# Kernel tuning notes

Measured on AMD Instinct MI355X. Metric: run time of the kernel, lower is better.

Reference implementation:

```python
import jax, jax.numpy as jnp
import numpy as np

N = 2048
NONGT = 2048
EMB = 64
GROUP = 16
FEAT = 256
DM = 1024  # dim[0] == dim[1]
DHEAD = DM // GROUP  # 64


def setup_inputs() -> dict:
    key = jax.random.key(0)
    ks = jax.random.split(key, 12)
    s = lambda fan_in: 1.0 / np.sqrt(fan_in)
    return {
        "roi_feat": jax.random.normal(ks[0], (N, FEAT), jnp.float32),
        "position_embedding": jax.random.uniform(ks[1], (N, NONGT, EMB), jnp.float32),
        "fc1_w": jax.random.normal(ks[2], (GROUP, EMB), jnp.float32) * s(EMB),
        "fc1_b": jnp.zeros((GROUP,), jnp.float32),
        "fc2_w": jax.random.normal(ks[3], (DM, FEAT), jnp.float32) * s(FEAT),
        "fc2_b": jnp.zeros((DM,), jnp.float32),
        "fc3_w": jax.random.normal(ks[4], (DM, FEAT), jnp.float32) * s(FEAT),
        "fc3_b": jnp.zeros((DM,), jnp.float32),
        "conv_w": jax.random.normal(ks[5], (FEAT, GROUP * FEAT), jnp.float32) * s(GROUP * FEAT),
        "conv_b": jnp.zeros((FEAT,), jnp.float32),
        "nongt_dim": NONGT,
    }


def reference(roi_feat, position_embedding, fc1_w, fc1_b, fc2_w, fc2_b,
              fc3_w, fc3_b, conv_w, conv_b, nongt_dim):
    nongt_roi_feat = roi_feat[:nongt_dim, :]                      # [M, FEAT]
    # position bias: relu(fc1(pe)) -> [N, M, G] -> [N, G, M]
    pos1 = jax.nn.relu(jnp.einsum('nme,ge->nmg', position_embedding, fc1_w) + fc1_b)
    aff_weight = jnp.transpose(pos1, (0, 2, 1))                   # [N, G, M]
    # grouped Q, K
    q = roi_feat @ fc2_w.T + fc2_b                                # [N, DM]
    q = q.reshape(-1, GROUP, DHEAD)                               # [N, G, d]
    k = nongt_roi_feat @ fc3_w.T + fc3_b                          # [M, DM]
    k = k.reshape(-1, GROUP, DHEAD)                               # [M, G, d]
    scale = 1.0 / np.sqrt(float(DHEAD))
    aff = jnp.einsum('ngd,mgd->ngm', q, k) * scale                # [N, G, M]
    weighted = jnp.log(jnp.maximum(aff_weight, 1e-6)) + aff
    aff_softmax = jax.nn.softmax(weighted, axis=-1)               # [N, G, M]
    out_t = jnp.einsum('ngm,mc->ngc', aff_softmax, nongt_roi_feat)  # [N, G, FEAT]
    flat = out_t.reshape(out_t.shape[0], GROUP * FEAT)            # channel order g*FEAT + c
    return flat @ conv_w.T + conv_b                               # [N, FEAT]
```

## Files before the change

### kernel.cpp

```cpp
#include <hip/hip_runtime.h>
#include <hip/hip_bf16.h>

#define NQ   2048
#define NK   2048
#define EMB  64
#define GRP  16
#define FEAT 256

typedef __bf16 bf16x8 __attribute__((ext_vector_type(8)));
typedef __bf16 bf16x4 __attribute__((ext_vector_type(4)));
typedef float  f32x4  __attribute__((ext_vector_type(4)));

#define MFMA(a, b, c) __builtin_amdgcn_mfma_f32_16x16x32_bf16((a), (b), (c), 0, 0, 0)

typedef __attribute__((address_space(3))) unsigned int  lds_u32;
typedef __attribute__((address_space(1))) unsigned int  glb_u32;

static __device__ __forceinline__ bf16x8 cvt8(float4 a, float4 b) {
    bf16x8 r;
    r[0] = (__bf16)a.x; r[1] = (__bf16)a.y; r[2] = (__bf16)a.z; r[3] = (__bf16)a.w;
    r[4] = (__bf16)b.x; r[5] = (__bf16)b.y; r[6] = (__bf16)b.z; r[7] = (__bf16)b.w;
    return r;
}

__launch_bounds__(256, 2)
__global__ void prep_all(const float* __restrict__ roi,
                         const float* __restrict__ pe,
                         const float* __restrict__ fc1w,
                         const float* __restrict__ fc1b,
                         const float* __restrict__ fc2w,
                         const float* __restrict__ fc2b,
                         const float* __restrict__ fc3w,
                         const float* __restrict__ fc3b,
                         const float* __restrict__ cw,
                         __bf16* __restrict__ roiT,
                         __bf16* __restrict__ convwb,
                         __bf16* __restrict__ qb,
                         __bf16* __restrict__ kb,
                         __bf16* __restrict__ wg) {
    __shared__ float tile[64][65];
    const int b   = blockIdx.x;
    const int tid = threadIdx.x;

    if (b < 128) {
        const int m0 = (b >> 2) * 64, c0 = (b & 3) * 64;
        const int tr = tid >> 4, tc = tid & 15;
#pragma unroll
        for (int ch = 0; ch < 4; ++ch) {
            int r = ch * 16 + tr;
            float4 v = *(const float4*)(roi + (m0 + r) * 256 + c0 + tc * 4);
            tile[r][tc * 4 + 0] = v.x; tile[r][tc * 4 + 1] = v.y;
            tile[r][tc * 4 + 2] = v.z; tile[r][tc * 4 + 3] = v.w;
        }
        __syncthreads();
#pragma unroll
        for (int ch = 0; ch < 4; ++ch) {
            int crow = ch * 16 + tr;
            int mm = tc * 4;
            bf16x4 o;
            o[0] = (__bf16)tile[mm + 0][crow]; o[1] = (__bf16)tile[mm + 1][crow];
            o[2] = (__bf16)tile[mm + 2][crow]; o[3] = (__bf16)tile[mm + 3][crow];
            *(bf16x4*)(roiT + (c0 + crow) * 2048 + m0 + mm) = o;
        }
    } else if (b < 640) {
        const int cb = b - 128;
        for (int i = cb * 256 + tid; i < 262144; i += 512 * 256) {
            float4 v = ((const float4*)cw)[i];
            bf16x4 o;
            o[0] = (__bf16)v.x; o[1] = (__bf16)v.y; o[2] = (__bf16)v.z; o[3] = (__bf16)v.w;
            ((bf16x4*)convwb)[i] = o;
        }
    } else if (b < 1664) {
        const int qi = b - 640;
        const int x  = qi & 511;
        const int isK = qi >> 9;
        const float* W    = isK ? fc3w : fc2w;
        const float* bias = isK ? fc3b : fc2b;
        __bf16*      out  = isK ? kb   : qb;
        const int l = tid & 63, wid = tid >> 6;
        const int n0 = (x >> 2) * 16;
        const int dmB = (x & 3) * 256 + wid * 64;
        const int lr = l & 15, lk = l >> 4;
        f32x4 acc[4];
#pragma unroll
        for (int i = 0; i < 4; ++i) acc[i] = (f32x4){0.f, 0.f, 0.f, 0.f};
        for (int k0 = 0; k0 < 256; k0 += 32) {
            const float* ap = roi + (n0 + lr) * 256 + k0 + lk * 8;
            bf16x8 af = cvt8(*(const float4*)ap, *(const float4*)(ap + 4));
#pragma unroll
            for (int cf = 0; cf < 4; ++cf) {
                const float* bp = W + (dmB + cf * 16 + lr) * 256 + k0 + lk * 8;
                acc[cf] = MFMA(af, cvt8(*(const float4*)bp, *(const float4*)(bp + 4)), acc[cf]);
            }
        }
#pragma unroll
        for (int cf = 0; cf < 4; ++cf) {
            int dm = dmB + cf * 16 + lr;
            float bv = bias[dm];
            int g = dm >> 6, d = dm & 63;
#pragma unroll
            for (int ri = 0; ri < 4; ++ri) {
                int n = n0 + lk * 4 + ri;
                out[(g * 2048 + n) * 64 + d] = (__bf16)(acc[cf][ri] + bv);
            }
        }
    } else {
        const int wb = b - 1664;
        const int l = tid & 63, wid = tid >> 6;
        const int lr = l & 15, lk = l >> 4;
        const long n = wb >> 2;
        const int mbase = (wb & 3) * 512 + wid * 128;

        bf16x8 fcB[2];
#pragma unroll
        for (int s = 0; s < 2; ++s) {
            const float* p = fc1w + lr * 64 + s * 32 + lk * 8;
            fcB[s] = cvt8(*(const float4*)p, *(const float4*)(p + 4));
        }
        const float bias = fc1b[lr];

        const float* pebase = pe + (n * 2048 + mbase + lr) * 64 + lk * 8;
        __bf16* obase = wg + (n * 16 + lr) * 2048 + mbase + lk * 4;

#pragma unroll 4
        for (int it = 0; it < 8; ++it) {
            const float* p0 = pebase + it * 16 * 64;
            f32x4 c = (f32x4){0.f, 0.f, 0.f, 0.f};
            c = MFMA(cvt8(*(const float4*)(p0),      *(const float4*)(p0 + 4)),  fcB[0], c);
            c = MFMA(cvt8(*(const float4*)(p0 + 32), *(const float4*)(p0 + 36)), fcB[1], c);
            bf16x4 o;
#pragma unroll
            for (int ri = 0; ri < 4; ++ri)
                o[ri] = (__bf16)fmaxf(fmaxf(c[ri] + bias, 0.f), 1e-6f);
            *(bf16x4*)(obase + it * 16) = o;
        }
    }
}

#define P_BASE 32768
__launch_bounds__(256, 2)
__global__ void relation_attn(const __bf16* __restrict__ wg,
                              const __bf16* __restrict__ qb,
                              const __bf16* __restrict__ kb,
                              const __bf16* __restrict__ roiT,
                              __bf16* __restrict__ flat) {
    __shared__ __align__(16) unsigned char smem[40960];
    const int tid = threadIdx.x;
    const int l   = tid & 63;
    const int wid = tid >> 6;
    const int s_  = ((blockIdx.x & 7) << 6) | (blockIdx.x >> 3);
    const int n0  = (s_ & 255) * 8;
    const int ghalf = s_ >> 8;
    const int lr  = l & 15;
    const int lk  = l >> 4;
    const int gh  = lk >> 1;
    const int nqh = lk & 1;
    const int g2  = ghalf * 8 + wid * 2;
    const int gA  = g2 + gh;

    bf16x8 qa[2][2];
#pragma unroll
    for (int gi = 0; gi < 2; ++gi)
#pragma unroll
        for (int s = 0; s < 2; ++s)
            qa[gi][s] = *(const bf16x8*)(qb + (long)((g2 + gi) * 2048 + n0 + (lr & 7)) * 64 + s * 32 + lk * 8);

    f32x4 acc[16];
#pragma unroll
    for (int i = 0; i < 16; ++i) acc[i] = (f32x4){0.f, 0.f, 0.f, 0.f};
    float dsum[4] = {0.f, 0.f, 0.f, 0.f};

    const __bf16* wptr = wg + (long)((n0 + (nqh << 2)) * 16 + gA) * 2048 + lr;

    for (int t = 0; t < 32; ++t) {
        const int m0t = t * 64;
        __syncthreads();

        {
            const int crow = l >> 3, slot = l & 7;
#pragma unroll
            for (int i = 0; i < 8; ++i) {
                int c = wid * 64 + i * 8 + crow;
                int D = slot ^ (c & 7);
                const __bf16* gp = roiT + c * 2048 + m0t + D * 8;
                __builtin_amdgcn_global_load_lds(
                    (const glb_u32*)(const void*)gp,
                    (lds_u32*)(void*)(smem + wid * 8192 + i * 1024), 16, 0, 0);
            }
        }

        float wlv[4][4];
#pragma unroll
        for (int mf = 0; mf < 4; ++mf)
#pragma unroll
            for (int ri = 0; ri < 4; ++ri)
                wlv[mf][ri] = (float)wptr[(long)ri * 32768 + m0t + mf * 16];

        __builtin_amdgcn_s_setprio(1);
        f32x4 a0[4], a1[4];
#pragma unroll
        for (int mf = 0; mf < 4; ++mf) {
            const __bf16* kp = kb + (long)(g2 * 2048 + m0t + mf * 16 + lr) * 64 + lk * 8;
            bf16x8 k0 = *(const bf16x8*)(kp);
            bf16x8 k1 = *(const bf16x8*)(kp + 32);
            f32x4 z = (f32x4){0.f, 0.f, 0.f, 0.f};
            z = MFMA(qa[0][0], k0, z);
            z = MFMA(qa[0][1], k1, z);
            a0[mf] = z;
        }
#pragma unroll
        for (int mf = 0; mf < 4; ++mf) {
            const __bf16* kp = kb + (long)((g2 + 1) * 2048 + m0t + mf * 16 + lr) * 64 + lk * 8;
            bf16x8 k0 = *(const bf16x8*)(kp);
            bf16x8 k1 = *(const bf16x8*)(kp + 32);
            f32x4 z = (f32x4){0.f, 0.f, 0.f, 0.f};
            z = MFMA(qa[1][0], k0, z);
            z = MFMA(qa[1][1], k1, z);
            a1[mf] = z;
        }
        __builtin_amdgcn_s_setprio(0);

#pragma unroll
        for (int mf = 0; mf < 4; ++mf) {
            int mm = mf * 16 + lr;
#pragma unroll
            for (int ri = 0; ri < 4; ++ri) {
                float a = gh ? a1[mf][ri] : a0[mf][ri];
                int n2 = (nqh << 2) + ri;
                float pv = wlv[mf][ri] * __expf(a * 0.125f);
                dsum[ri] += pv;
                int rp = ((gA & 7) << 3) + n2;
                int poff = (rp << 7) + ((mm ^ (n2 << 3)) << 1);
                *(__bf16*)(smem + P_BASE + poff) = (__bf16)pv;
            }
        }

        __syncthreads();

        {
            const int rpA = wid * 16 + lr;
            const int QA = (rpA & 7) << 3;
            __builtin_amdgcn_s_setprio(1);
#pragma unroll
            for (int s = 0; s < 2; ++s) {
                bf16x8 pA = *(const bf16x8*)(smem + P_BASE + (rpA << 7)
                                             + (((s * 32 + lk * 8) ^ QA) << 1));
#pragma unroll
                for (int cf = 0; cf < 16; ++cf) {
                    int c = cf * 16 + lr;
                    bf16x8 rB = *(const bf16x8*)(smem + c * 128
                                                 + (((s * 4 + lk) ^ (c & 7)) << 4));
                    acc[cf] = MFMA(pA, rB, acc[cf]);
                }
            }
            __builtin_amdgcn_s_setprio(0);
        }
    }

    float inv[4];
#pragma unroll
    for (int ri = 0; ri < 4; ++ri) {
        float v = dsum[ri];
        v += __shfl_xor(v, 1); v += __shfl_xor(v, 2);
        v += __shfl_xor(v, 4); v += __shfl_xor(v, 8);
        inv[ri] = 1.0f / v;
    }
#pragma unroll
    for (int cf = 0; cf < 16; ++cf) {
        int c = cf * 16 + lr;
#pragma unroll
        for (int ri = 0; ri < 4; ++ri) {
            int n2 = (nqh << 2) + ri;
            flat[(long)(n0 + n2) * 4096 + gA * 256 + c] = (__bf16)(acc[cf][ri] * inv[ri]);
        }
    }
}

__launch_bounds__(256)
__global__ void conv_gemm(const __bf16* __restrict__ flat, const __bf16* __restrict__ cw,
                          const float* __restrict__ cb, float* __restrict__ out) {
    const int tid = threadIdx.x, l = tid & 63, wid = tid >> 6;
    const int n0 = (blockIdx.x >> 1) * 16;
    const int j0 = (blockIdx.x & 1) * 128 + wid * 32;
    const int lr = l & 15, lk = l >> 4;
    f32x4 acc[2] = {(f32x4){0.f, 0.f, 0.f, 0.f}, (f32x4){0.f, 0.f, 0.f, 0.f}};
#pragma unroll 4
    for (int k0 = 0; k0 < 4096; k0 += 32) {
        bf16x8 af = *(const bf16x8*)(flat + (long)(n0 + lr) * 4096 + k0 + lk * 8);
#pragma unroll
        for (int cf = 0; cf < 2; ++cf) {
            bf16x8 bfr = *(const bf16x8*)(cw + (long)(j0 + cf * 16 + lr) * 4096 + k0 + lk * 8);
            acc[cf] = MFMA(af, bfr, acc[cf]);
        }
    }
#pragma unroll
    for (int cf = 0; cf < 2; ++cf) {
        int j = j0 + cf * 16 + lr;
        float bv = cb[j];
#pragma unroll
        for (int ri = 0; ri < 4; ++ri)
            out[(n0 + lk * 4 + ri) * 256 + j] = acc[cf][ri] + bv;
    }
}

extern "C" void kernel_launch(void* const* d_in, const int* in_sizes, int n_in,
                              void* d_out, int out_size, void* d_ws, size_t ws_size,
                              hipStream_t stream) {
    const float* roi  = (const float*)d_in[0];
    const float* pe   = (const float*)d_in[1];
    const float* fc1w = (const float*)d_in[2];
    const float* fc1b = (const float*)d_in[3];
    const float* fc2w = (const float*)d_in[4];
    const float* fc2b = (const float*)d_in[5];
    const float* fc3w = (const float*)d_in[6];
    const float* fc3b = (const float*)d_in[7];
    const float* cw   = (const float*)d_in[8];
    const float* cb   = (const float*)d_in[9];
    float* out = (float*)d_out;

    unsigned char* ws = (unsigned char*)d_ws;
    __bf16* roiT   = (__bf16*)(ws);
    __bf16* convwb = (__bf16*)(ws + (1ull  << 20));
    __bf16* qb     = (__bf16*)(ws + (3ull  << 20));
    __bf16* kb     = (__bf16*)(ws + (7ull  << 20));
    __bf16* flat   = (__bf16*)(ws + (11ull << 20));
    __bf16* wg     = (__bf16*)(ws + (27ull << 20));

    prep_all<<<9856, 256, 0, stream>>>(roi, pe, fc1w, fc1b, fc2w, fc2b,
                                       fc3w, fc3b, cw,
                                       roiT, convwb, qb, kb, wg);
    relation_attn<<<512, 256, 0, stream>>>(wg, qb, kb, roiT, flat);
    conv_gemm<<<256, 256, 0, stream>>>(flat, convwb, cb, out);
}
```

Before: 489.6 us.

## Fuse position-embedding fc1 into attention kernel and drop wg intermediate

Removes the separate pass that turned position_embedding into a bf16 weight tensor wg in global memory. The attention kernel now computes relu(fc1(pe)) itself into an LDS buffer, prefetching the next tile's pe during the current tile's work. Blocks grow to 512 threads covering all 16 groups for 8 queries, so each pe row is read once per query block. This saves the wg write and read-back (about 128 MB of bf16 traffic). The cost is a grid of only 256 blocks with 64KB of LDS each, which may lower occupancy and latency hiding on the 1GB pe stream.

```diff
diff --git a/kernel.cpp b/kernel.cpp
--- a/kernel.cpp
+++ b/kernel.cpp
@@ -24,20 +24,16 @@
 }
 
 __launch_bounds__(256, 2)
-__global__ void prep_all(const float* __restrict__ roi,
-                         const float* __restrict__ pe,
-                         const float* __restrict__ fc1w,
-                         const float* __restrict__ fc1b,
-                         const float* __restrict__ fc2w,
-                         const float* __restrict__ fc2b,
-                         const float* __restrict__ fc3w,
-                         const float* __restrict__ fc3b,
-                         const float* __restrict__ cw,
-                         __bf16* __restrict__ roiT,
-                         __bf16* __restrict__ convwb,
-                         __bf16* __restrict__ qb,
-                         __bf16* __restrict__ kb,
-                         __bf16* __restrict__ wg) {
+__global__ void prep_small(const float* __restrict__ roi,
+                           const float* __restrict__ fc2w,
+                           const float* __restrict__ fc2b,
+                           const float* __restrict__ fc3w,
+                           const float* __restrict__ fc3b,
+                           const float* __restrict__ cw,
+                           __bf16* __restrict__ roiT,
+                           __bf16* __restrict__ convwb,
+                           __bf16* __restrict__ qb,
+                           __bf16* __restrict__ kb) {
     __shared__ float tile[64][65];
     const int b   = blockIdx.x;
     const int tid = threadIdx.x;
@@ -70,7 +66,7 @@
             o[0] = (__bf16)v.x; o[1] = (__bf16)v.y; o[2] = (__bf16)v.z; o[3] = (__bf16)v.w;
             ((bf16x4*)convwb)[i] = o;
         }
-    } else if (b < 1664) {
+    } else {
         const int qi = b - 640;
         const int x  = qi & 511;
         const int isK = qi >> 9;
@@ -104,58 +100,29 @@
                 out[(g * 2048 + n) * 64 + d] = (__bf16)(acc[cf][ri] + bv);
             }
         }
-    } else {
-        const int wb = b - 1664;
-        const int l = tid & 63, wid = tid >> 6;
-        const int lr = l & 15, lk = l >> 4;
-        const long n = wb >> 2;
-        const int mbase = (wb & 3) * 512 + wid * 128;
-
-        bf16x8 fcB[2];
-#pragma unroll
-        for (int s = 0; s < 2; ++s) {
-            const float* p = fc1w + lr * 64 + s * 32 + lk * 8;
-            fcB[s] = cvt8(*(const float4*)p, *(const float4*)(p + 4));
-        }
-        const float bias = fc1b[lr];
-
-        const float* pebase = pe + (n * 2048 + mbase + lr) * 64 + lk * 8;
-        __bf16* obase = wg + (n * 16 + lr) * 2048 + mbase + lk * 4;
-
-#pragma unroll 4
-        for (int it = 0; it < 8; ++it) {
-            const float* p0 = pebase + it * 16 * 64;
-            f32x4 c = (f32x4){0.f, 0.f, 0.f, 0.f};
-            c = MFMA(cvt8(*(const float4*)(p0),      *(const float4*)(p0 + 4)),  fcB[0], c);
-            c = MFMA(cvt8(*(const float4*)(p0 + 32), *(const float4*)(p0 + 36)), fcB[1], c);
-            bf16x4 o;
-#pragma unroll
-            for (int ri = 0; ri < 4; ++ri)
-                o[ri] = (__bf16)fmaxf(fmaxf(c[ri] + bias, 0.f), 1e-6f);
-            *(bf16x4*)(obase + it * 16) = o;
-        }
     }
 }
 
 #define P_BASE 32768
-__launch_bounds__(256, 2)
-__global__ void relation_attn(const __bf16* __restrict__ wg,
-                              const __bf16* __restrict__ qb,
-                              const __bf16* __restrict__ kb,
-                              const __bf16* __restrict__ roiT,
-                              __bf16* __restrict__ flat) {
-    __shared__ __align__(16) unsigned char smem[40960];
+#define W_BASE 49152
+__launch_bounds__(512, 2)
+__global__ void mega(const float* __restrict__ pe,
+                     const float* __restrict__ fc1w,
+                     const float* __restrict__ fc1b,
+                     const __bf16* __restrict__ qb,
+                     const __bf16* __restrict__ kb,
+                     const __bf16* __restrict__ roiT,
+                     __bf16* __restrict__ flat) {
+    __shared__ __align__(16) unsigned char smem[65536];
     const int tid = threadIdx.x;
     const int l   = tid & 63;
     const int wid = tid >> 6;
-    const int s_  = ((blockIdx.x & 7) << 6) | (blockIdx.x >> 3);
-    const int n0  = (s_ & 255) * 8;
-    const int ghalf = s_ >> 8;
+    const int n0  = blockIdx.x * 8;
     const int lr  = l & 15;
     const int lk  = l >> 4;
     const int gh  = lk >> 1;
     const int nqh = lk & 1;
-    const int g2  = ghalf * 8 + wid * 2;
+    const int g2  = wid * 2;
     const int gA  = g2 + gh;
 
     bf16x8 qa[2][2];
@@ -165,12 +132,37 @@
         for (int s = 0; s < 2; ++s)
             qa[gi][s] = *(const bf16x8*)(qb + (long)((g2 + gi) * 2048 + n0 + (lr & 7)) * 64 + s * 32 + lk * 8);
 
+    bf16x8 fcB[2];
+#pragma unroll
+    for (int s = 0; s < 2; ++s) {
+        const float* p = fc1w + lr * 64 + s * 32 + lk * 8;
+        fcB[s] = cvt8(*(const float4*)p, *(const float4*)(p + 4));
+    }
+    const float wbias = fc1b[lr];
+
     f32x4 acc[16];
 #pragma unroll
     for (int i = 0; i < 16; ++i) acc[i] = (f32x4){0.f, 0.f, 0.f, 0.f};
     float dsum[4] = {0.f, 0.f, 0.f, 0.f};
 
-    const __bf16* wptr = wg + (long)((n0 + (nqh << 2)) * 16 + gA) * 2048 + lr;
+    const float* pewave = pe + ((long)(n0 + wid) * 2048) * 64;
+
+    {
+#pragma unroll
+        for (int mf = 0; mf < 4; ++mf) {
+            const float* pr = pewave + (mf * 16 + lr) * 64 + lk * 8;
+            f32x4 c = (f32x4){0.f, 0.f, 0.f, 0.f};
+            c = MFMA(cvt8(*(const float4*)(pr),      *(const float4*)(pr + 4)),  fcB[0], c);
+            c = MFMA(cvt8(*(const float4*)(pr + 32), *(const float4*)(pr + 36)), fcB[1], c);
+            bf16x4 o;
+#pragma unroll
+            for (int ri = 0; ri < 4; ++ri)
+                o[ri] = (__bf16)fmaxf(fmaxf(c[ri] + wbias, 0.f), 1e-6f);
+            int woff = W_BASE + (lr * 8 + wid) * 128
+                     + ((((mf << 1) + (lk >> 1)) ^ (lr & 7)) << 4) + ((lk & 1) << 3);
+            *(bf16x4*)(smem + woff) = o;
+        }
+    }
 
     for (int t = 0; t < 32; ++t) {
         const int m0t = t * 64;
@@ -179,46 +171,54 @@
         {
             const int crow = l >> 3, slot = l & 7;
 #pragma unroll
-            for (int i = 0; i < 8; ++i) {
-                int c = wid * 64 + i * 8 + crow;
+            for (int i = 0; i < 4; ++i) {
+                int c = wid * 32 + i * 8 + crow;
                 int D = slot ^ (c & 7);
                 const __bf16* gp = roiT + c * 2048 + m0t + D * 8;
                 __builtin_amdgcn_global_load_lds(
                     (const glb_u32*)(const void*)gp,
-                    (lds_u32*)(void*)(smem + wid * 8192 + i * 1024), 16, 0, 0);
-            }
-        }
-
-        float wlv[4][4];
-#pragma unroll
-        for (int mf = 0; mf < 4; ++mf)
-#pragma unroll
-            for (int ri = 0; ri < 4; ++ri)
-                wlv[mf][ri] = (float)wptr[(long)ri * 32768 + m0t + mf * 16];
-
-        __builtin_amdgcn_s_setprio(1);
+                    (lds_u32*)(void*)(smem + wid * 4096 + i * 1024), 16, 0, 0);
+            }
+        }
+
+        bf16x8 kf[2][4][2];
+#pragma unroll
+        for (int gi = 0; gi < 2; ++gi)
+#pragma unroll
+            for (int mf = 0; mf < 4; ++mf) {
+                const __bf16* kp = kb + (long)((g2 + gi) * 2048 + m0t + mf * 16 + lr) * 64 + lk * 8;
+                kf[gi][mf][0] = *(const bf16x8*)(kp);
+                kf[gi][mf][1] = *(const bf16x8*)(kp + 32);
+            }
+
+        float4 pev[4][2][2];
+        if (t < 31) {
+            const float* pt = pewave + (long)(m0t + 64) * 64;
+#pragma unroll
+            for (int mf = 0; mf < 4; ++mf)
+#pragma unroll
+                for (int s = 0; s < 2; ++s) {
+                    const float* pp = pt + (mf * 16 + lr) * 64 + s * 32 + lk * 8;
+                    pev[mf][s][0] = *(const float4*)pp;
+                    pev[mf][s][1] = *(const float4*)(pp + 4);
+                }
+        }
+
         f32x4 a0[4], a1[4];
 #pragma unroll
         for (int mf = 0; mf < 4; ++mf) {
-            const __bf16* kp = kb + (long)(g2 * 2048 + m0t + mf * 16 + lr) * 64 + lk * 8;
-            bf16x8 k0 = *(const bf16x8*)(kp);
-            bf16x8 k1 = *(const bf16x8*)(kp + 32);
             f32x4 z = (f32x4){0.f, 0.f, 0.f, 0.f};
-            z = MFMA(qa[0][0], k0, z);
-            z = MFMA(qa[0][1], k1, z);
+            z = MFMA(qa[0][0], kf[0][mf][0], z);
+            z = MFMA(qa[0][1], kf[0][mf][1], z);
             a0[mf] = z;
         }
 #pragma unroll
         for (int mf = 0; mf < 4; ++mf) {
-            const __bf16* kp = kb + (long)((g2 + 1) * 2048 + m0t + mf * 16 + lr) * 64 + lk * 8;
-            bf16x8 k0 = *(const bf16x8*)(kp);
-            bf16x8 k1 = *(const bf16x8*)(kp + 32);
             f32x4 z = (f32x4){0.f, 0.f, 0.f, 0.f};
-            z = MFMA(qa[1][0], k0, z);
-            z = MFMA(qa[1][1], k1, z);
+            z = MFMA(qa[1][0], kf[1][mf][0], z);
+            z = MFMA(qa[1][1], kf[1][mf][1], z);
             a1[mf] = z;
         }
-        __builtin_amdgcn_s_setprio(0);
 
 #pragma unroll
         for (int mf = 0; mf < 4; ++mf) {
@@ -227,9 +227,13 @@
             for (int ri = 0; ri < 4; ++ri) {
                 float a = gh ? a1[mf][ri] : a0[mf][ri];
                 int n2 = (nqh << 2) + ri;
-                float pv = wlv[mf][ri] * __expf(a * 0.125f);
+                int wrow = (gA << 3) + n2;
+                int wslot = ((mf << 1) + (lr >> 3)) ^ (gA & 7);
+                float wv = (float)*(const __bf16*)(smem + W_BASE + (wrow << 7)
+                                                   + (wslot << 4) + ((mm & 7) << 1));
+                float pv = wv * __expf(a * 0.125f);
                 dsum[ri] += pv;
-                int rp = ((gA & 7) << 3) + n2;
+                int rp = (gA << 3) + n2;
                 int poff = (rp << 7) + ((mm ^ (n2 << 3)) << 1);
                 *(__bf16*)(smem + P_BASE + poff) = (__bf16)pv;
             }
@@ -240,7 +244,6 @@
         {
             const int rpA = wid * 16 + lr;
             const int QA = (rpA & 7) << 3;
-            __builtin_amdgcn_s_setprio(1);
 #pragma unroll
             for (int s = 0; s < 2; ++s) {
                 bf16x8 pA = *(const bf16x8*)(smem + P_BASE + (rpA << 7)
@@ -253,7 +256,22 @@
                     acc[cf] = MFMA(pA, rB, acc[cf]);
                 }
             }
-            __builtin_amdgcn_s_setprio(0);
+        }
+
+        if (t < 31) {
+#pragma unroll
+            for (int mf = 0; mf < 4; ++mf) {
+                f32x4 c = (f32x4){0.f, 0.f, 0.f, 0.f};
+                c = MFMA(cvt8(pev[mf][0][0], pev[mf][0][1]), fcB[0], c);
+                c = MFMA(cvt8(pev[mf][1][0], pev[mf][1][1]), fcB[1], c);
+                bf16x4 o;
+#pragma unroll
+                for (int ri = 0; ri < 4; ++ri)
+                    o[ri] = (__bf16)fmaxf(fmaxf(c[ri] + wbias, 0.f), 1e-6f);
+                int woff = W_BASE + (lr * 8 + wid) * 128
+                         + ((((mf << 1) + (lk >> 1)) ^ (lr & 7)) << 4) + ((lk & 1) << 3);
+                *(bf16x4*)(smem + woff) = o;
+            }
         }
     }
 
@@ -324,11 +342,9 @@
     __bf16* qb     = (__bf16*)(ws + (3ull  << 20));
     __bf16* kb     = (__bf16*)(ws + (7ull  << 20));
     __bf16* flat   = (__bf16*)(ws + (11ull << 20));
-    __bf16* wg     = (__bf16*)(ws + (27ull << 20));
-
-    prep_all<<<9856, 256, 0, stream>>>(roi, pe, fc1w, fc1b, fc2w, fc2b,
-                                       fc3w, fc3b, cw,
-                                       roiT, convwb, qb, kb, wg);
-    relation_attn<<<512, 256, 0, stream>>>(wg, qb, kb, roiT, flat);
+
+    prep_small<<<1664, 256, 0, stream>>>(roi, fc2w, fc2b, fc3w, fc3b, cw,
+                                         roiT, convwb, qb, kb);
+    mega<<<256, 512, 0, stream>>>(pe, fc1w, fc1b, qb, kb, roiT, flat);
     conv_gemm<<<256, 256, 0, stream>>>(flat, convwb, cb, out);
 }
```

Measured after the change: 532.3 us. 1.09x slower.

## Split fused attention into QK/softmax-numerator kernel and separate PV GEMM

Applied to the files above, without the earlier changes.

The fused relation_attn kernel is split in two. The first kernel computes the unnormalized softmax numerators and writes them to a full 16x2048x2048 bf16 matrix in global memory, plus per-row inverse sums. A second kernel then runs a plain GEMM of that matrix against roiT and scales by the inverse sums. This removes the LDS staging and the two barriers per tile from the fused loop, but adds a 128 MB round trip through global memory and an extra launch.

```diff
diff --git a/kernel.cpp b/kernel.cpp
--- a/kernel.cpp
+++ b/kernel.cpp
@@ -137,14 +137,12 @@
     }
 }
 
-#define P_BASE 32768
 __launch_bounds__(256, 2)
-__global__ void relation_attn(const __bf16* __restrict__ wg,
-                              const __bf16* __restrict__ qb,
-                              const __bf16* __restrict__ kb,
-                              const __bf16* __restrict__ roiT,
-                              __bf16* __restrict__ flat) {
-    __shared__ __align__(16) unsigned char smem[40960];
+__global__ void qk_extract(const __bf16* __restrict__ wg,
+                           const __bf16* __restrict__ qb,
+                           const __bf16* __restrict__ kb,
+                           __bf16* __restrict__ pmat,
+                           float* __restrict__ invb) {
     const int tid = threadIdx.x;
     const int l   = tid & 63;
     const int wid = tid >> 6;
@@ -165,29 +163,13 @@
         for (int s = 0; s < 2; ++s)
             qa[gi][s] = *(const bf16x8*)(qb + (long)((g2 + gi) * 2048 + n0 + (lr & 7)) * 64 + s * 32 + lk * 8);
 
-    f32x4 acc[16];
-#pragma unroll
-    for (int i = 0; i < 16; ++i) acc[i] = (f32x4){0.f, 0.f, 0.f, 0.f};
     float dsum[4] = {0.f, 0.f, 0.f, 0.f};
 
     const __bf16* wptr = wg + (long)((n0 + (nqh << 2)) * 16 + gA) * 2048 + lr;
+    __bf16* pbase = pmat + ((long)gA * 2048 + n0 + (nqh << 2)) * 2048 + lr;
 
     for (int t = 0; t < 32; ++t) {
         const int m0t = t * 64;
-        __syncthreads();
-
-        {
-            const int crow = l >> 3, slot = l & 7;
-#pragma unroll
-            for (int i = 0; i < 8; ++i) {
-                int c = wid * 64 + i * 8 + crow;
-                int D = slot ^ (c & 7);
-                const __bf16* gp = roiT + c * 2048 + m0t + D * 8;
-                __builtin_amdgcn_global_load_lds(
-                    (const glb_u32*)(const void*)gp,
-                    (lds_u32*)(void*)(smem + wid * 8192 + i * 1024), 16, 0, 0);
-            }
-        }
 
         float wlv[4][4];
 #pragma unroll
@@ -222,56 +204,56 @@
 
 #pragma unroll
         for (int mf = 0; mf < 4; ++mf) {
-            int mm = mf * 16 + lr;
 #pragma unroll
             for (int ri = 0; ri < 4; ++ri) {
                 float a = gh ? a1[mf][ri] : a0[mf][ri];
-                int n2 = (nqh << 2) + ri;
                 float pv = wlv[mf][ri] * __expf(a * 0.125f);
                 dsum[ri] += pv;
-                int rp = ((gA & 7) << 3) + n2;
-                int poff = (rp << 7) + ((mm ^ (n2 << 3)) << 1);
-                *(__bf16*)(smem + P_BASE + poff) = (__bf16)pv;
+                pbase[(long)ri * 2048 + m0t + mf * 16] = (__bf16)pv;
             }
         }
-
-        __syncthreads();
-
-        {
-            const int rpA = wid * 16 + lr;
-            const int QA = (rpA & 7) << 3;
-            __builtin_amdgcn_s_setprio(1);
-#pragma unroll
-            for (int s = 0; s < 2; ++s) {
-                bf16x8 pA = *(const bf16x8*)(smem + P_BASE + (rpA << 7)
-                                             + (((s * 32 + lk * 8) ^ QA) << 1));
-#pragma unroll
-                for (int cf = 0; cf < 16; ++cf) {
-                    int c = cf * 16 + lr;
-                    bf16x8 rB = *(const bf16x8*)(smem + c * 128
-                                                 + (((s * 4 + lk) ^ (c & 7)) << 4));
-                    acc[cf] = MFMA(pA, rB, acc[cf]);
-                }
-            }
-            __builtin_amdgcn_s_setprio(0);
-        }
-    }
-
-    float inv[4];
+    }
+
 #pragma unroll
     for (int ri = 0; ri < 4; ++ri) {
         float v = dsum[ri];
         v += __shfl_xor(v, 1); v += __shfl_xor(v, 2);
         v += __shfl_xor(v, 4); v += __shfl_xor(v, 8);
-        inv[ri] = 1.0f / v;
-    }
-#pragma unroll
-    for (int cf = 0; cf < 16; ++cf) {
-        int c = cf * 16 + lr;
+        if (lr == 0)
+            invb[(n0 + (nqh << 2) + ri) * 16 + gA] = 1.0f / v;
+    }
+}
+
+__launch_bounds__(256)
+__global__ void pv_gemm(const __bf16* __restrict__ pmat,
+                        const __bf16* __restrict__ roiT,
+                        const float* __restrict__ invb,
+                        __bf16* __restrict__ flat) {
+    const int tid = threadIdx.x, l = tid & 63, wid = tid >> 6;
+    const int g  = blockIdx.x & 15;
+    const int nb = (blockIdx.x >> 4) & 127;
+    const int ch = blockIdx.x >> 11;
+    const int n0 = nb * 16;
+    const int j0 = ch * 128 + wid * 32;
+    const int lr = l & 15, lk = l >> 4;
+    f32x4 acc[2] = {(f32x4){0.f, 0.f, 0.f, 0.f}, (f32x4){0.f, 0.f, 0.f, 0.f}};
+    const __bf16* pA = pmat + ((long)g * 2048 + n0 + lr) * 2048 + lk * 8;
+#pragma unroll 4
+    for (int k0 = 0; k0 < 2048; k0 += 32) {
+        bf16x8 af = *(const bf16x8*)(pA + k0);
+#pragma unroll
+        for (int cf = 0; cf < 2; ++cf) {
+            bf16x8 bfr = *(const bf16x8*)(roiT + (long)(j0 + cf * 16 + lr) * 2048 + k0 + lk * 8);
+            acc[cf] = MFMA(af, bfr, acc[cf]);
+        }
+    }
+#pragma unroll
+    for (int cf = 0; cf < 2; ++cf) {
+        int j = j0 + cf * 16 + lr;
 #pragma unroll
         for (int ri = 0; ri < 4; ++ri) {
-            int n2 = (nqh << 2) + ri;
-            flat[(long)(n0 + n2) * 4096 + gA * 256 + c] = (__bf16)(acc[cf][ri] * inv[ri]);
+            int n = n0 + lk * 4 + ri;
+            flat[(long)n * 4096 + g * 256 + j] = (__bf16)(acc[cf][ri] * invb[n * 16 + g]);
         }
     }
 }
@@ -325,10 +307,13 @@
     __bf16* kb     = (__bf16*)(ws + (7ull  << 20));
     __bf16* flat   = (__bf16*)(ws + (11ull << 20));
     __bf16* wg     = (__bf16*)(ws + (27ull << 20));
+    __bf16* pmat   = (__bf16*)(ws + (160ull << 20));
+    float*  invb   = (float*) (ws + (292ull << 20));
 
     prep_all<<<9856, 256, 0, stream>>>(roi, pe, fc1w, fc1b, fc2w, fc2b,
                                        fc3w, fc3b, cw,
                                        roiT, convwb, qb, kb, wg);
-    relation_attn<<<512, 256, 0, stream>>>(wg, qb, kb, roiT, flat);
+    qk_extract<<<512, 256, 0, stream>>>(wg, qb, kb, pmat, invb);
+    pv_gemm<<<4096, 256, 0, stream>>>(pmat, roiT, invb, flat);
     conv_gemm<<<256, 256, 0, stream>>>(flat, convwb, cb, out);
 }
```

Result: slower. 834.6 us (+70.5%).

## Warp-specialize attention kernel into producer and consumer waves with double-buffered LDS

Applied to the files above, without the earlier changes.

Grows relation_attn to 512 threads. Four producer waves compute the QK scores, exp weights and row sums, and issue the roi tile loads into LDS. Four consumer waves run the P·roi MFMA accumulation, with both the P tile and the roi tile double-buffered, so score computation for tile t+1 overlaps the PV matmul for tile t. The softmax denominators are passed through LDS to the consumer waves for the final scaling. This doubles LDS per block to 80KB, and the two wave roles must hit matched barrier counts.

```diff
diff --git a/kernel.cpp b/kernel.cpp
--- a/kernel.cpp
+++ b/kernel.cpp
@@ -137,14 +137,16 @@
     }
 }
 
-#define P_BASE 32768
-__launch_bounds__(256, 2)
+#define ROI_BUF 32768
+#define P_OFF   65536
+#define P_BUF   8192
+__launch_bounds__(512, 2)
 __global__ void relation_attn(const __bf16* __restrict__ wg,
                               const __bf16* __restrict__ qb,
                               const __bf16* __restrict__ kb,
                               const __bf16* __restrict__ roiT,
                               __bf16* __restrict__ flat) {
-    __shared__ __align__(16) unsigned char smem[40960];
+    __shared__ __align__(16) unsigned char smem[81920];
     const int tid = threadIdx.x;
     const int l   = tid & 63;
     const int wid = tid >> 6;
@@ -155,123 +157,140 @@
     const int lk  = l >> 4;
     const int gh  = lk >> 1;
     const int nqh = lk & 1;
-    const int g2  = ghalf * 8 + wid * 2;
-    const int gA  = g2 + gh;
-
-    bf16x8 qa[2][2];
-#pragma unroll
-    for (int gi = 0; gi < 2; ++gi)
-#pragma unroll
-        for (int s = 0; s < 2; ++s)
-            qa[gi][s] = *(const bf16x8*)(qb + (long)((g2 + gi) * 2048 + n0 + (lr & 7)) * 64 + s * 32 + lk * 8);
-
-    f32x4 acc[16];
-#pragma unroll
-    for (int i = 0; i < 16; ++i) acc[i] = (f32x4){0.f, 0.f, 0.f, 0.f};
-    float dsum[4] = {0.f, 0.f, 0.f, 0.f};
-
-    const __bf16* wptr = wg + (long)((n0 + (nqh << 2)) * 16 + gA) * 2048 + lr;
-
-    for (int t = 0; t < 32; ++t) {
-        const int m0t = t * 64;
+
+    if (wid < 4) {
+        const int pw = wid;
+        const int g2 = ghalf * 8 + pw * 2;
+        const int gA = g2 + gh;
+
+        bf16x8 qa[2][2];
+#pragma unroll
+        for (int gi = 0; gi < 2; ++gi)
+#pragma unroll
+            for (int s = 0; s < 2; ++s)
+                qa[gi][s] = *(const bf16x8*)(qb + (long)((g2 + gi) * 2048 + n0 + (lr & 7)) * 64 + s * 32 + lk * 8);
+
+        float dsum[4] = {0.f, 0.f, 0.f, 0.f};
+        const __bf16* wptr = wg + (long)((n0 + (nqh << 2)) * 16 + gA) * 2048 + lr;
+
+        for (int pt = 0; pt < 32; ++pt) {
+            const int m0  = pt * 64;
+            const int buf = pt & 1;
+
+            {
+                const int crow = l >> 3, slot = l & 7;
+#pragma unroll
+                for (int i = 0; i < 8; ++i) {
+                    int c = pw * 64 + i * 8 + crow;
+                    int D = slot ^ (c & 7);
+                    const __bf16* gp = roiT + c * 2048 + m0 + D * 8;
+                    __builtin_amdgcn_global_load_lds(
+                        (const glb_u32*)(const void*)gp,
+                        (lds_u32*)(void*)(smem + buf * ROI_BUF + pw * 8192 + i * 1024), 16, 0, 0);
+                }
+            }
+
+            float wlv[4][4];
+#pragma unroll
+            for (int mf = 0; mf < 4; ++mf)
+#pragma unroll
+                for (int ri = 0; ri < 4; ++ri)
+                    wlv[mf][ri] = (float)wptr[(long)ri * 32768 + m0 + mf * 16];
+
+            __builtin_amdgcn_s_setprio(1);
+            f32x4 a0[4], a1[4];
+#pragma unroll
+            for (int mf = 0; mf < 4; ++mf) {
+                const __bf16* kp = kb + (long)(g2 * 2048 + m0 + mf * 16 + lr) * 64 + lk * 8;
+                bf16x8 k0 = *(const bf16x8*)(kp);
+                bf16x8 k1 = *(const bf16x8*)(kp + 32);
+                f32x4 z = (f32x4){0.f, 0.f, 0.f, 0.f};
+                z = MFMA(qa[0][0], k0, z);
+                z = MFMA(qa[0][1], k1, z);
+                a0[mf] = z;
+            }
+#pragma unroll
+            for (int mf = 0; mf < 4; ++mf) {
+                const __bf16* kp = kb + (long)((g2 + 1) * 2048 + m0 + mf * 16 + lr) * 64 + lk * 8;
+                bf16x8 k0 = *(const bf16x8*)(kp);
+                bf16x8 k1 = *(const bf16x8*)(kp + 32);
+                f32x4 z = (f32x4){0.f, 0.f, 0.f, 0.f};
+                z = MFMA(qa[1][0], k0, z);
+                z = MFMA(qa[1][1], k1, z);
+                a1[mf] = z;
+            }
+            __builtin_amdgcn_s_setprio(0);
+
+#pragma unroll
+            for (int mf = 0; mf < 4; ++mf) {
+                int mm = mf * 16 + lr;
+#pragma unroll
+                for (int ri = 0; ri < 4; ++ri) {
+                    float a = gh ? a1[mf][ri] : a0[mf][ri];
+                    int n2 = (nqh << 2) + ri;
+                    float pv = wlv[mf][ri] * __expf(a * 0.125f);
+                    dsum[ri] += pv;
+                    int rp = ((gA & 7) << 3) + n2;
+                    int poff = P_OFF + buf * P_BUF + (rp << 7) + ((mm ^ (n2 << 3)) << 1);
+                    *(__bf16*)(smem + poff) = (__bf16)pv;
+                }
+            }
+
+            __syncthreads();
+        }
+
+        {
+            float* invl = (float*)(smem + P_OFF);
+#pragma unroll
+            for (int ri = 0; ri < 4; ++ri) {
+                float v = dsum[ri];
+                v += __shfl_xor(v, 1); v += __shfl_xor(v, 2);
+                v += __shfl_xor(v, 4); v += __shfl_xor(v, 8);
+                if (lr == 0)
+                    invl[(((pw << 1) + gh) << 3) + (nqh << 2) + ri] = 1.0f / v;
+            }
+        }
         __syncthreads();
-
-        {
-            const int crow = l >> 3, slot = l & 7;
-#pragma unroll
-            for (int i = 0; i < 8; ++i) {
-                int c = wid * 64 + i * 8 + crow;
-                int D = slot ^ (c & 7);
-                const __bf16* gp = roiT + c * 2048 + m0t + D * 8;
-                __builtin_amdgcn_global_load_lds(
-                    (const glb_u32*)(const void*)gp,
-                    (lds_u32*)(void*)(smem + wid * 8192 + i * 1024), 16, 0, 0);
-            }
-        }
-
-        float wlv[4][4];
-#pragma unroll
-        for (int mf = 0; mf < 4; ++mf)
-#pragma unroll
-            for (int ri = 0; ri < 4; ++ri)
-                wlv[mf][ri] = (float)wptr[(long)ri * 32768 + m0t + mf * 16];
-
-        __builtin_amdgcn_s_setprio(1);
-        f32x4 a0[4], a1[4];
-#pragma unroll
-        for (int mf = 0; mf < 4; ++mf) {
-            const __bf16* kp = kb + (long)(g2 * 2048 + m0t + mf * 16 + lr) * 64 + lk * 8;
-            bf16x8 k0 = *(const bf16x8*)(kp);
-            bf16x8 k1 = *(const bf16x8*)(kp + 32);
-            f32x4 z = (f32x4){0.f, 0.f, 0.f, 0.f};
-            z = MFMA(qa[0][0], k0, z);
-            z = MFMA(qa[0][1], k1, z);
-            a0[mf] = z;
-        }
-#pragma unroll
-        for (int mf = 0; mf < 4; ++mf) {
-            const __bf16* kp = kb + (long)((g2 + 1) * 2048 + m0t + mf * 16 + lr) * 64 + lk * 8;
-            bf16x8 k0 = *(const bf16x8*)(kp);
-            bf16x8 k1 = *(const bf16x8*)(kp + 32);
-            f32x4 z = (f32x4){0.f, 0.f, 0.f, 0.f};
-            z = MFMA(qa[1][0], k0, z);
-            z = MFMA(qa[1][1], k1, z);
-            a1[mf] = z;
-        }
-        __builtin_amdgcn_s_setprio(0);
-
-#pragma unroll
-        for (int mf = 0; mf < 4; ++mf) {
-            int mm = mf * 16 + lr;
-#pragma unroll
-            for (int ri = 0; ri < 4; ++ri) {
-                float a = gh ? a1[mf][ri] : a0[mf][ri];
-                int n2 = (nqh << 2) + ri;
-                float pv = wlv[mf][ri] * __expf(a * 0.125f);
-                dsum[ri] += pv;
-                int rp = ((gA & 7) << 3) + n2;
-                int poff = (rp << 7) + ((mm ^ (n2 << 3)) << 1);
-                *(__bf16*)(smem + P_BASE + poff) = (__bf16)pv;
-            }
-        }
+    } else {
+        const int cw = wid & 3;
+        f32x4 acc[16];
+#pragma unroll
+        for (int i = 0; i < 16; ++i) acc[i] = (f32x4){0.f, 0.f, 0.f, 0.f};
 
         __syncthreads();
 
-        {
-            const int rpA = wid * 16 + lr;
+        for (int t = 0; t < 32; ++t) {
+            const int buf = t & 1;
+            const int rpA = cw * 16 + lr;
             const int QA = (rpA & 7) << 3;
             __builtin_amdgcn_s_setprio(1);
 #pragma unroll
             for (int s = 0; s < 2; ++s) {
-                bf16x8 pA = *(const bf16x8*)(smem + P_BASE + (rpA << 7)
+                bf16x8 pA = *(const bf16x8*)(smem + P_OFF + buf * P_BUF + (rpA << 7)
                                              + (((s * 32 + lk * 8) ^ QA) << 1));
 #pragma unroll
                 for (int cf = 0; cf < 16; ++cf) {
                     int c = cf * 16 + lr;
-                    bf16x8 rB = *(const bf16x8*)(smem + c * 128
+                    bf16x8 rB = *(const bf16x8*)(smem + buf * ROI_BUF + c * 128
                                                  + (((s * 4 + lk) ^ (c & 7)) << 4));
                     acc[cf] = MFMA(pA, rB, acc[cf]);
                 }
             }
             __builtin_amdgcn_s_setprio(0);
-        }
-    }
-
-    float inv[4];
-#pragma unroll
-    for (int ri = 0; ri < 4; ++ri) {
-        float v = dsum[ri];
-        v += __shfl_xor(v, 1); v += __shfl_xor(v, 2);
-        v += __shfl_xor(v, 4); v += __shfl_xor(v, 8);
-        inv[ri] = 1.0f / v;
-    }
-#pragma unroll
-    for (int cf = 0; cf < 16; ++cf) {
-        int c = cf * 16 + lr;
-#pragma unroll
-        for (int ri = 0; ri < 4; ++ri) {
-            int n2 = (nqh << 2) + ri;
-            flat[(long)(n0 + n2) * 4096 + gA * 256 + c] = (__bf16)(acc[cf][ri] * inv[ri]);
+            __syncthreads();
+        }
+
+        const float* invl = (const float*)(smem + P_OFF);
+        const int glo = (cw << 1) + gh;
+#pragma unroll
+        for (int cf = 0; cf < 16; ++cf) {
+            int c = cf * 16 + lr;
+#pragma unroll
+            for (int ri = 0; ri < 4; ++ri) {
+                int n2 = (nqh << 2) + ri;
+                flat[(long)(n0 + n2) * 4096 + (ghalf * 8 + glo) * 256 + c]
+                    = (__bf16)(acc[cf][ri] * invl[(glo << 3) + n2]);
+            }
         }
     }
 }
@@ -329,6 +348,6 @@
     prep_all<<<9856, 256, 0, stream>>>(roi, pe, fc1w, fc1b, fc2w, fc2b,
                                        fc3w, fc3b, cw,
                                        roiT, convwb, qb, kb, wg);
-    relation_attn<<<512, 256, 0, stream>>>(wg, qb, kb, roiT, flat);
+    relation_attn<<<512, 512, 0, stream>>>(wg, qb, kb, roiT, flat);
     conv_gemm<<<256, 256, 0, stream>>>(flat, convwb, cb, out);
 }
```

New measurement: 504.8 us. +3.1%, slower.
